# Performance work log

Measured on AMD Instinct MI355X. Metric: run time of the kernel, lower is better.

The kernel has to match this reference:

```python
import jax, jax.numpy as jnp
import numpy as np

GH, GW = 7, 7            # hierarchical grid size
LN_EPS = 1e-5            # torch nn.LayerNorm default eps
NEG = -1e9


def _adaptive_avg_pool2d(x, oh, ow):
    # Replicates torch F.adaptive_avg_pool2d bin boundaries:
    # start=floor(i*H/out), end=ceil((i+1)*H/out). x: (..., H, W)
    H, W = x.shape[-2], x.shape[-1]
    def b(i, n, o):
        return int(np.floor(i * n / o)), int(np.ceil((i + 1) * n / o))
    rows = jnp.stack([x[..., b(i, H, oh)[0]:b(i, H, oh)[1], :].mean(axis=-2)
                      for i in range(oh)], axis=-2)
    out = jnp.stack([rows[..., b(j, W, ow)[0]:b(j, W, ow)[1]].mean(axis=-1)
                     for j in range(ow)], axis=-1)
    return out


def _layernorm(y, gamma, beta):
    mu = y.mean(axis=-1, keepdims=True)
    var = jnp.mean(jnp.square(y - mu), axis=-1, keepdims=True)
    return (y - mu) * jax.lax.rsqrt(var + LN_EPS) * gamma + beta


def setup_inputs() -> dict:
    key = jax.random.key(0)
    ks = jax.random.split(key, 16)
    B, C, H, W = 8, 512, 32, 32
    heads = 8
    s = 0.02
    f32 = jnp.float32
    return {
        "x":    jax.random.normal(ks[0], (B, C, H, W), f32),
        "Wq":   jax.random.normal(ks[1], (C, C), f32) * s,
        "bq":   jnp.zeros((C,), f32),
        "Wk":   jax.random.normal(ks[2], (C, C), f32) * s,
        "bk":   jnp.zeros((C,), f32),
        "Wv":   jax.random.normal(ks[3], (C, C), f32) * s,
        "bv":   jnp.zeros((C,), f32),
        "Wo":   jax.random.normal(ks[4], (C, C), f32) * s,
        "bo":   jnp.zeros((C,), f32),
        "Wsp":  jax.random.normal(ks[5], (heads, C), f32) * s,   # 1x1 conv C->heads
        "bsp":  jnp.zeros((heads,), f32),
        "Wse1": jax.random.normal(ks[6], (C // 16, C), f32) * s, # SE squeeze
        "bse1": jnp.zeros((C // 16,), f32),
        "Wse2": jax.random.normal(ks[7], (C, C // 16), f32) * s, # SE excite
        "bse2": jnp.zeros((C,), f32),
        "gamma": jnp.ones((C,), f32),
        "beta":  jnp.zeros((C,), f32),
    }


def reference(x, Wq, bq, Wk, bk, Wv, bv, Wo, bo, Wsp, bsp,
              Wse1, bse1, Wse2, bse2, gamma, beta):
    B, C, H, W = x.shape
    heads = Wsp.shape[0]
    d = C // heads
    N = H * W

    # --- hierarchical grid mask ---
    sp = jnp.einsum('bchw,nc->bnhw', x, Wsp) + bsp[None, :, None, None]
    m = jax.nn.sigmoid(sp)                               # (B, heads, H, W)
    mg = _adaptive_avg_pool2d(m, GH, GW)
    mg = (mg > 0.5).astype(x.dtype)                      # binarize
    ih = np.floor(np.arange(H) * GH / H).astype(np.int32)  # torch 'nearest'
    iw = np.floor(np.arange(W) * GW / W).astype(np.int32)
    mask = mg[..., ih[:, None], iw[None, :]]             # (B, heads, H, W)

    # --- SE channel gating ---
    pooled = x.mean(axis=(2, 3))                         # (B, C)
    h1 = jax.nn.relu(pooled @ Wse1.T + bse1)
    cw = jax.nn.sigmoid(h1 @ Wse2.T + bse2)              # (B, C)
    xf = (x * cw[:, :, None, None]).reshape(B, C, N).transpose(0, 2, 1)  # (B,N,C)

    # --- multi-head attention with outer-product additive mask ---
    def heads_split(t):
        return t.reshape(B, N, heads, d).transpose(0, 2, 1, 3)  # (B,h,N,d)
    Q = heads_split(xf @ Wq.T + bq)
    K = heads_split(xf @ Wk.T + bk)
    V = heads_split(xf @ Wv.T + bv)

    scores = jnp.einsum('bhnd,bhmd->bhnm', Q, K) / (d ** 0.5)
    mf = mask.reshape(B, heads, N)
    bias = (1.0 - mf[:, :, :, None] * mf[:, :, None, :]) * NEG
    w = jax.nn.softmax(scores + bias, axis=-1)
    attn = jnp.einsum('bhnm,bhmd->bhnd', w, V)
    attn = attn.transpose(0, 2, 1, 3).reshape(B, N, C)
    attn = attn @ Wo.T + bo

    y = _layernorm(xf + attn, gamma, beta)               # (B, N, C)
    return y.transpose(0, 2, 1).reshape(B, C, H, W)
```

## Files before the change

kernel.cpp:

```cpp
#include <hip/hip_runtime.h>
#include <hip/hip_bf16.h>
#include <math.h>

typedef unsigned short u16;
typedef unsigned int u32;
typedef __attribute__((ext_vector_type(4))) float f32x4;
typedef __attribute__((ext_vector_type(8))) short bf16x8;
typedef __attribute__((ext_vector_type(4))) unsigned short us4;
typedef __attribute__((ext_vector_type(8))) unsigned short us8;

#define DI __device__ __forceinline__

#define NEGS  (-1.4426950408889634e9f)
#define QKSCL (0.18033688011112042f)
#define DEFTH (11.541560327111708f)

DI u16 f2b(float x){ __hip_bfloat16 h = __float2bfloat16(x); return *reinterpret_cast<u16*>(&h); }
DI float b2f(u16 u){ union { float f; u32 i; } v; v.i = ((u32)u) << 16; return v.f; }

DI u32 cvtpk(float lo, float hi){
  u32 r;
  asm("v_cvt_pk_bf16_f32 %0, %1, %2" : "=v"(r) : "v"(lo), "v"(hi));
  return r;
}
DI float exp2a(float x){
  float r;
  asm("v_exp_f32 %0, %1" : "=v"(r) : "v"(x));
  return r;
}

DI void gload16(const void* g, void* l){
  __builtin_amdgcn_global_load_lds((const __attribute__((address_space(1))) void*)g,
                                   (__attribute__((address_space(3))) void*)l, 16, 0, 0);
}

__global__ void k_cvt(const float* __restrict__ Wq, const float* __restrict__ Wk,
                      const float* __restrict__ Wv, const float* __restrict__ Wo,
                      u16* __restrict__ WB, u16* __restrict__ WoB){
  int i = blockIdx.x * 256 + threadIdx.x;
  WB[i]          = f2b(Wq[i]);
  WB[262144 + i] = f2b(Wk[i]);
  WB[524288 + i] = f2b(Wv[i]);
  WoB[i]         = f2b(Wo[i]);
}

__global__ __launch_bounds__(256) void k_pooled(const float* __restrict__ x, float* __restrict__ pooled){
  int row  = blockIdx.x * 4 + (threadIdx.x >> 6);
  int lane = threadIdx.x & 63;
  const float4* p = (const float4*)(x + ((size_t)row << 10));
  float4 v0 = p[lane], v1 = p[lane + 64], v2 = p[lane + 128], v3 = p[lane + 192];
  float s = (v0.x + v0.y + v0.z + v0.w) + (v1.x + v1.y + v1.z + v1.w)
          + (v2.x + v2.y + v2.z + v2.w) + (v3.x + v3.y + v3.z + v3.w);
  #pragma unroll
  for (int o = 32; o > 0; o >>= 1) s += __shfl_down(s, o, 64);
  if (lane == 0) pooled[row] = s * (1.0f / 1024.0f);
}

__global__ __launch_bounds__(256) void k_se(const float* __restrict__ pooled,
    const float* __restrict__ Wse1, const float* __restrict__ bse1,
    const float* __restrict__ Wse2, const float* __restrict__ bse2,
    float* __restrict__ cw){
  __shared__ float pl[512];
  __shared__ float h1[32];
  int b = blockIdx.x, t = threadIdx.x;
  pl[t] = pooled[b * 512 + t];
  pl[t + 256] = pooled[b * 512 + t + 256];
  __syncthreads();
  if (t < 32){
    float acc = bse1[t];
    const float* w = Wse1 + t * 512;
    for (int c = 0; c < 512; c++) acc = fmaf(pl[c], w[c], acc);
    h1[t] = fmaxf(acc, 0.0f);
  }
  __syncthreads();
  for (int c = t; c < 512; c += 256){
    float acc = bse2[c];
    const float* w = Wse2 + c * 32;
    #pragma unroll
    for (int j = 0; j < 32; j++) acc = fmaf(h1[j], w[j], acc);
    cw[b * 512 + c] = 1.0f / (1.0f + expf(-acc));
  }
}

__global__ __launch_bounds__(256) void k_spxf(const float* __restrict__ x,
    const float* __restrict__ Wsp, const float* __restrict__ bsp,
    const float* __restrict__ cw, float* __restrict__ mbuf, u16* __restrict__ xfB){
  __shared__ float wsh[4096];
  __shared__ float cwl[512];
  __shared__ float tile[64][36];
  __shared__ float part[8][256];
  int t = threadIdx.x;
  int b = blockIdx.x >> 5, n0 = (blockIdx.x & 31) << 5;
  for (int i = t; i < 4096; i += 256) wsh[i] = Wsp[i];
  cwl[t] = cw[b * 512 + t];
  cwl[t + 256] = cw[b * 512 + t + 256];

  int nl = t & 31, cg = t >> 5;
  int lr = t >> 2, lc = (t & 3) << 3;
  float acc[8] = {0,0,0,0,0,0,0,0};

  for (int cb = 0; cb < 8; cb++){
    __syncthreads();
    const float* xp = x + ((size_t)(b * 512 + cb * 64 + lr) << 10) + n0 + lc;
    float4 v0 = *(const float4*)xp;
    float4 v1 = *(const float4*)(xp + 4);
    *(float4*)&tile[lr][lc]     = v0;
    *(float4*)&tile[lr][lc + 4] = v1;
    __syncthreads();
    float sc[8];
    #pragma unroll
    for (int i = 0; i < 8; i++){
      int c = cb * 64 + cg * 8 + i;
      float v = tile[cg * 8 + i][nl];
      sc[i] = v * cwl[c];
      #pragma unroll
      for (int h = 0; h < 8; h++) acc[h] = fmaf(v, wsh[(h << 9) + c], acc[h]);
    }
    union { u32 d[4]; us8 v; } xu;
    #pragma unroll
    for (int i = 0; i < 4; i++) xu.d[i] = cvtpk(sc[2*i], sc[2*i+1]);
    *(us8*)&xfB[(((size_t)(b * 1024 + n0 + nl)) << 9) + cb * 64 + cg * 8] = xu.v;
  }
  #pragma unroll
  for (int h = 0; h < 8; h++) part[cg][h * 32 + nl] = acc[h];
  __syncthreads();
  {
    int h = t >> 5, px = t & 31;
    float s = bsp[h];
    #pragma unroll
    for (int g2 = 0; g2 < 8; g2++) s += part[g2][h * 32 + px];
    mbuf[(((size_t)(b * 8 + h)) << 10) + n0 + px] = 1.0f / (1.0f + expf(-s));
  }
}

__global__ void k_mask(const float* __restrict__ mbuf, float* __restrict__ bneg){
  __shared__ float sm[1024];
  __shared__ float mg[49];
  int bh = blockIdx.x, t = threadIdx.x;
  const float* mp = mbuf + ((size_t)bh << 10);
  for (int i = t; i < 1024; i += 64) sm[i] = mp[i];
  __syncthreads();
  if (t < 49){
    int ci = t / 7, cj = t % 7;
    int r0 = (ci * 32) / 7, r1 = ((ci + 1) * 32 + 6) / 7;
    int c0 = (cj * 32) / 7, c1 = ((cj + 1) * 32 + 6) / 7;
    float acc = 0.0f;
    for (int cc = c0; cc < c1; cc++){
      float rs = 0.0f;
      for (int rr = r0; rr < r1; rr++) rs += sm[rr * 32 + cc];
      acc += rs / (float)(r1 - r0);
    }
    float v = acc / (float)(c1 - c0);
    mg[t] = (v > 0.5f) ? 1.0f : 0.0f;
  }
  __syncthreads();
  for (int i = t; i < 1024; i += 64){
    int r = i >> 5, c = i & 31;
    float m = mg[((r * 7) >> 5) * 7 + ((c * 7) >> 5)];
    bneg[((size_t)bh << 10) + i] = (m > 0.5f) ? 0.0f : NEGS;
  }
}

template<int MODE>
DI void gemm_body(const u16* __restrict__ A, const u16* __restrict__ Bw,
    const float* __restrict__ b0, const float* __restrict__ b1, const float* __restrict__ b2,
    u16* __restrict__ outQ, u16* __restrict__ outK, u16* __restrict__ outV, u16* __restrict__ outO){
  __shared__ __align__(16) u16 smem[16384];
  int m0 = blockIdx.x * 128, n0 = blockIdx.y * 128;
  bool vblk = (MODE == 0) && (n0 >= 1024);
  int t = threadIdx.x, lane = t & 63, w = t >> 6;
  int wr = w >> 1, wc = w & 1;
  int g = lane >> 4, li = lane & 15;
  f32x4 acc[4][4];
  #pragma unroll
  for (int mt = 0; mt < 4; mt++)
    #pragma unroll
    for (int nt = 0; nt < 4; nt++) acc[mt][nt] = (f32x4){0.f, 0.f, 0.f, 0.f};

  int cof = (((lane & 3) ^ ((lane >> 3) & 3)) << 3);
  int rl = lane >> 2;
  const u16* gA = A  + (size_t)(m0 + w * 32 + rl) * 512 + cof;
  const u16* gB = Bw + (size_t)(n0 + w * 32 + rl) * 512 + cof;
  u16* lA = smem + (w * 32) * 32;
  u16* lB = smem + 4096 + (w * 32) * 32;

  #define STAGE(buf, k0)                                              \
    gload16(gA + (k0),            lA + (buf) * 8192);                 \
    gload16(gA + (k0) + 16 * 512, lA + (buf) * 8192 + 512);           \
    gload16(gB + (k0),            lB + (buf) * 8192);                 \
    gload16(gB + (k0) + 16 * 512, lB + (buf) * 8192 + 512);

  STAGE(0, 0);
  __syncthreads();

  int rsw = ((li >> 1) & 3);
  int cA = (g ^ rsw) << 3;
  int cur = 0;
  for (int ks = 0; ks < 16; ks++){
    if (ks < 15){ STAGE(cur ^ 1, (ks + 1) * 32); }
    const u16* Ac = smem + cur * 8192;
    const u16* Bc = smem + cur * 8192 + 4096;
    bf16x8 afr[4], bfr[4];
    #pragma unroll
    for (int mt = 0; mt < 4; mt++)
      afr[mt] = *(const bf16x8*)&Ac[(wr * 64 + mt * 16 + li) * 32 + cA];
    #pragma unroll
    for (int nt = 0; nt < 4; nt++)
      bfr[nt] = *(const bf16x8*)&Bc[(wc * 64 + nt * 16 + li) * 32 + cA];
    if (vblk){
      #pragma unroll
      for (int mt = 0; mt < 4; mt++)
        #pragma unroll
        for (int nt = 0; nt < 4; nt++)
          acc[mt][nt] = __builtin_amdgcn_mfma_f32_16x16x32_bf16(afr[mt], bfr[nt], acc[mt][nt], 0, 0, 0);
    } else {
      #pragma unroll
      for (int mt = 0; mt < 4; mt++)
        #pragma unroll
        for (int nt = 0; nt < 4; nt++)
          acc[mt][nt] = __builtin_amdgcn_mfma_f32_16x16x32_bf16(bfr[nt], afr[mt], acc[mt][nt], 0, 0, 0);
    }
    __syncthreads();
    cur ^= 1;
  }
  #undef STAGE

  u16* Cl = smem;
  const float* bb = vblk ? b2 : ((MODE == 0 && (n0 >> 9)) ? b1 : b0);
  #pragma unroll
  for (int p = 0; p < 2; p++){
    __syncthreads();
    if (vblk){
      if (wc == p){
        #pragma unroll
        for (int mt = 0; mt < 4; mt++){
          #pragma unroll
          for (int nt = 0; nt < 4; nt++){
            int row = nt * 16 + li;
            float bias = bb[(n0 & 511) + p * 64 + row];
            int col = wr * 64 + ((mt >> 1) << 5) + (g << 3) + ((mt & 1) << 2);
            union { u32 d[2]; us4 v; } pu;
            pu.d[0] = cvtpk(acc[mt][nt][0] + bias, acc[mt][nt][1] + bias);
            pu.d[1] = cvtpk(acc[mt][nt][2] + bias, acc[mt][nt][3] + bias);
            *(us4*)&Cl[row * 136 + col] = pu.v;
          }
        }
      }
    } else {
      if (wr == p){
        #pragma unroll
        for (int mt = 0; mt < 4; mt++){
          #pragma unroll
          for (int nt = 0; nt < 4; nt++){
            int row = mt * 16 + li;
            int ob = wc * 64 + nt * 16 + (g << 2);
            float4 bias4 = *(const float4*)&bb[(n0 & 511) + ob];
            union { u32 d[2]; us4 v; } pu;
            pu.d[0] = cvtpk(acc[mt][nt][0] + bias4.x, acc[mt][nt][1] + bias4.y);
            pu.d[1] = cvtpk(acc[mt][nt][2] + bias4.z, acc[mt][nt][3] + bias4.w);
            *(us4*)&Cl[row * 136 + ob] = pu.v;
          }
        }
      }
    }
    __syncthreads();
    int r = t >> 4, ol = (t & 15) << 3;
    if (vblk){
      int b = m0 >> 10, nt0 = m0 & 1023;
      #pragma unroll
      for (int pp = 0; pp < 4; pp++){
        int rr = pp * 16 + r;
        int c = (n0 & 511) + p * 64 + rr, h = c >> 6, dv = c & 63;
        us8 v = *(us8*)&Cl[rr * 136 + ol];
        *(us8*)&outV[(((size_t)(b * 8 + h)) << 16) + ((size_t)dv << 10) + nt0 + ol] = v;
      }
    } else if (MODE == 0){
      u16* base = (n0 >> 9) ? outK : outQ;
      #pragma unroll
      for (int pp = 0; pp < 4; pp++){
        int rr = pp * 16 + r;
        int m = m0 + p * 64 + rr, b = m >> 10, n = m & 1023;
        int c = (n0 & 511) + ol, h = c >> 6, dv = c & 63;
        us8 v = *(us8*)&Cl[rr * 136 + ol];
        *(us8*)&base[(((size_t)(b * 8 + h)) << 16) + ((size_t)n << 6) + dv] = v;
      }
    } else {
      #pragma unroll
      for (int pp = 0; pp < 4; pp++){
        int rr = pp * 16 + r;
        int m = m0 + p * 64 + rr;
        us8 v = *(us8*)&Cl[rr * 136 + ol];
        *(us8*)&outO[((size_t)m << 9) + n0 + ol] = v;
      }
    }
  }
}

__global__ __launch_bounds__(256) void k_gemm_qkv(const u16* __restrict__ A, const u16* __restrict__ Bw,
    const float* __restrict__ b0, const float* __restrict__ b1, const float* __restrict__ b2,
    u16* __restrict__ outQ, u16* __restrict__ outK, u16* __restrict__ outV){
  gemm_body<0>(A, Bw, b0, b1, b2, outQ, outK, outV, nullptr);
}

__global__ __launch_bounds__(256) void k_gemm_o(const u16* __restrict__ A, const u16* __restrict__ Bw,
    const float* __restrict__ b0, u16* __restrict__ outO){
  gemm_body<1>(A, Bw, b0, nullptr, nullptr, nullptr, nullptr, nullptr, outO);
}

__global__ __launch_bounds__(256) void k_flash(const u16* __restrict__ Q, const u16* __restrict__ K,
    const u16* __restrict__ Vt, const float* __restrict__ bneg, u16* __restrict__ attnB){
  __shared__ __align__(16) u16 Ks[2][64 * 88];
  __shared__ __align__(16) u16 Vts[2][64 * 88];
  __shared__ float mks[2][64];
  int hw = blockIdx.x;
  int bid = ((hw & 7) << 6) + (hw >> 3);
  int bh = bid >> 3, q0 = (bid & 7) << 7;
  int t = threadIdx.x, lane = t & 63, w = t >> 6;
  int g = lane >> 4, li = lane & 15;

  const u16* Kp = K  + ((size_t)bh << 16);
  const u16* Vp = Vt + ((size_t)bh << 16);
  const float* bp = bneg + ((size_t)bh << 10);

  bf16x8 qf0a, qf1a, qf0b, qf1b;
  {
    const u16* qra = Q + ((size_t)bh << 16) + ((size_t)(q0 + w * 32 + li) << 6);
    qf0a = *(const bf16x8*)(qra + g * 8);
    qf1a = *(const bf16x8*)(qra + 32 + g * 8);
    const u16* qrb = qra + (16 << 6);
    qf0b = *(const bf16x8*)(qrb + g * 8);
    qf1b = *(const bf16x8*)(qrb + 32 + g * 8);
  }
  float bnqa = bp[q0 + w * 32 + li];
  float bnqb = bp[q0 + w * 32 + 16 + li];

  f32x4 oaccA[4], oaccB[4];
  #pragma unroll
  for (int dt = 0; dt < 4; dt++){
    oaccA[dt] = (f32x4){0.f, 0.f, 0.f, 0.f};
    oaccB[dt] = (f32x4){0.f, 0.f, 0.f, 0.f};
  }
  float mrunA = -INFINITY, lrunA = 0.0f, mrunB = -INFINITY, lrunB = 0.0f;

  int sr = t >> 2, sc = (t & 3) << 4;
  const u16* kg = Kp + ((size_t)sr << 6) + sc;
  const u16* vg = Vp + ((size_t)sr << 10) + sc;
  uint4 kr0 = *(const uint4*)(kg), kr1 = *(const uint4*)(kg + 8);
  uint4 vr0 = *(const uint4*)(vg), vr1 = *(const uint4*)(vg + 8);
  float mr = (t < 64) ? bp[t] : 0.0f;

  *(uint4*)&Ks[0][sr * 88 + sc]      = kr0;
  *(uint4*)&Ks[0][sr * 88 + sc + 8]  = kr1;
  *(uint4*)&Vts[0][sr * 88 + sc]     = vr0;
  *(uint4*)&Vts[0][sr * 88 + sc + 8] = vr1;
  if (t < 64) mks[0][t] = mr;
  __syncthreads();

  for (int kt = 0; kt < 16; kt++){
    int buf = kt & 1;
    if (kt < 15){
      kr0 = *(const uint4*)(kg + (kt + 1) * 4096);
      kr1 = *(const uint4*)(kg + (kt + 1) * 4096 + 8);
      vr0 = *(const uint4*)(vg + (kt + 1) * 64);
      vr1 = *(const uint4*)(vg + (kt + 1) * 64 + 8);
      if (t < 64) mr = bp[(kt + 1) * 64 + t];
    }

    f32x4 sa[4], sb[4];
    #pragma unroll
    for (int mt = 0; mt < 4; mt++){ sa[mt] = (f32x4){0.f,0.f,0.f,0.f}; sb[mt] = (f32x4){0.f,0.f,0.f,0.f}; }
    __builtin_amdgcn_s_setprio(1);
    #pragma unroll
    for (int mt = 0; mt < 4; mt++){
      bf16x8 kf0 = *(bf16x8*)&Ks[buf][(mt * 16 + li) * 88 + g * 8];
      bf16x8 kf1 = *(bf16x8*)&Ks[buf][(mt * 16 + li) * 88 + 32 + g * 8];
      sa[mt] = __builtin_amdgcn_mfma_f32_16x16x32_bf16(kf0, qf0a, sa[mt], 0, 0, 0);
      sa[mt] = __builtin_amdgcn_mfma_f32_16x16x32_bf16(kf1, qf1a, sa[mt], 0, 0, 0);
      sb[mt] = __builtin_amdgcn_mfma_f32_16x16x32_bf16(kf0, qf0b, sb[mt], 0, 0, 0);
      sb[mt] = __builtin_amdgcn_mfma_f32_16x16x32_bf16(kf1, qf1b, sb[mt], 0, 0, 0);
    }
    __builtin_amdgcn_s_setprio(0);

    union { u32 d[4]; bf16x8 v; } u0a, u1a, u0b, u1b;
    {
      float tm[4];
      #pragma unroll
      for (int mt = 0; mt < 4; mt++){
        float4 bk = *(const float4*)&mks[buf][mt * 16 + g * 4];
        float s0 = fmaf(sa[mt][0], QKSCL, fminf(bk.x, bnqa));
        float s1 = fmaf(sa[mt][1], QKSCL, fminf(bk.y, bnqa));
        float s2 = fmaf(sa[mt][2], QKSCL, fminf(bk.z, bnqa));
        float s3 = fmaf(sa[mt][3], QKSCL, fminf(bk.w, bnqa));
        sa[mt][0] = s0; sa[mt][1] = s1; sa[mt][2] = s2; sa[mt][3] = s3;
        tm[mt] = fmaxf(fmaxf(s0, s1), fmaxf(s2, s3));
      }
      float tmax = fmaxf(fmaxf(tm[0], tm[1]), fmaxf(tm[2], tm[3]));
      tmax = fmaxf(tmax, __shfl_xor(tmax, 16, 64));
      tmax = fmaxf(tmax, __shfl_xor(tmax, 32, 64));
      if (!__all(tmax <= mrunA + DEFTH)){
        float mnew = fmaxf(mrunA, tmax);
        float scl = exp2a(mrunA - mnew);
        mrunA = mnew; lrunA *= scl;
        #pragma unroll
        for (int dt = 0; dt < 4; dt++)
          #pragma unroll
          for (int j = 0; j < 4; j++) oaccA[dt][j] *= scl;
      }
      float rs[4];
      #pragma unroll
      for (int mt = 0; mt < 4; mt++){
        float p0 = exp2a(sa[mt][0] - mrunA);
        float p1 = exp2a(sa[mt][1] - mrunA);
        float p2 = exp2a(sa[mt][2] - mrunA);
        float p3 = exp2a(sa[mt][3] - mrunA);
        sa[mt][0] = p0; sa[mt][1] = p1; sa[mt][2] = p2; sa[mt][3] = p3;
        rs[mt] = (p0 + p1) + (p2 + p3);
      }
      float rsum = (rs[0] + rs[1]) + (rs[2] + rs[3]);
      rsum += __shfl_xor(rsum, 16, 64);
      rsum += __shfl_xor(rsum, 32, 64);
      lrunA += rsum;
      u0a.d[0] = cvtpk(sa[0][0], sa[0][1]); u0a.d[1] = cvtpk(sa[0][2], sa[0][3]);
      u0a.d[2] = cvtpk(sa[1][0], sa[1][1]); u0a.d[3] = cvtpk(sa[1][2], sa[1][3]);
      u1a.d[0] = cvtpk(sa[2][0], sa[2][1]); u1a.d[1] = cvtpk(sa[2][2], sa[2][3]);
      u1a.d[2] = cvtpk(sa[3][0], sa[3][1]); u1a.d[3] = cvtpk(sa[3][2], sa[3][3]);
    }
    {
      float tm[4];
      #pragma unroll
      for (int mt = 0; mt < 4; mt++){
        float4 bk = *(const float4*)&mks[buf][mt * 16 + g * 4];
        float s0 = fmaf(sb[mt][0], QKSCL, fminf(bk.x, bnqb));
        float s1 = fmaf(sb[mt][1], QKSCL, fminf(bk.y, bnqb));
        float s2 = fmaf(sb[mt][2], QKSCL, fminf(bk.z, bnqb));
        float s3 = fmaf(sb[mt][3], QKSCL, fminf(bk.w, bnqb));
        sb[mt][0] = s0; sb[mt][1] = s1; sb[mt][2] = s2; sb[mt][3] = s3;
        tm[mt] = fmaxf(fmaxf(s0, s1), fmaxf(s2, s3));
      }
      float tmax = fmaxf(fmaxf(tm[0], tm[1]), fmaxf(tm[2], tm[3]));
      tmax = fmaxf(tmax, __shfl_xor(tmax, 16, 64));
      tmax = fmaxf(tmax, __shfl_xor(tmax, 32, 64));
      if (!__all(tmax <= mrunB + DEFTH)){
        float mnew = fmaxf(mrunB, tmax);
        float scl = exp2a(mrunB - mnew);
        mrunB = mnew; lrunB *= scl;
        #pragma unroll
        for (int dt = 0; dt < 4; dt++)
          #pragma unroll
          for (int j = 0; j < 4; j++) oaccB[dt][j] *= scl;
      }
      float rs[4];
      #pragma unroll
      for (int mt = 0; mt < 4; mt++){
        float p0 = exp2a(sb[mt][0] - mrunB);
        float p1 = exp2a(sb[mt][1] - mrunB);
        float p2 = exp2a(sb[mt][2] - mrunB);
        float p3 = exp2a(sb[mt][3] - mrunB);
        sb[mt][0] = p0; sb[mt][1] = p1; sb[mt][2] = p2; sb[mt][3] = p3;
        rs[mt] = (p0 + p1) + (p2 + p3);
      }
      float rsum = (rs[0] + rs[1]) + (rs[2] + rs[3]);
      rsum += __shfl_xor(rsum, 16, 64);
      rsum += __shfl_xor(rsum, 32, 64);
      lrunB += rsum;
      u0b.d[0] = cvtpk(sb[0][0], sb[0][1]); u0b.d[1] = cvtpk(sb[0][2], sb[0][3]);
      u0b.d[2] = cvtpk(sb[1][0], sb[1][1]); u0b.d[3] = cvtpk(sb[1][2], sb[1][3]);
      u1b.d[0] = cvtpk(sb[2][0], sb[2][1]); u1b.d[1] = cvtpk(sb[2][2], sb[2][3]);
      u1b.d[2] = cvtpk(sb[3][0], sb[3][1]); u1b.d[3] = cvtpk(sb[3][2], sb[3][3]);
    }

    __builtin_amdgcn_s_setprio(1);
    #pragma unroll
    for (int dt = 0; dt < 4; dt++){
      bf16x8 vf0 = *(bf16x8*)&Vts[buf][(dt * 16 + li) * 88 + g * 8];
      bf16x8 vf1 = *(bf16x8*)&Vts[buf][(dt * 16 + li) * 88 + 32 + g * 8];
      oaccA[dt] = __builtin_amdgcn_mfma_f32_16x16x32_bf16(vf0, u0a.v, oaccA[dt], 0, 0, 0);
      oaccA[dt] = __builtin_amdgcn_mfma_f32_16x16x32_bf16(vf1, u1a.v, oaccA[dt], 0, 0, 0);
      oaccB[dt] = __builtin_amdgcn_mfma_f32_16x16x32_bf16(vf0, u0b.v, oaccB[dt], 0, 0, 0);
      oaccB[dt] = __builtin_amdgcn_mfma_f32_16x16x32_bf16(vf1, u1b.v, oaccB[dt], 0, 0, 0);
    }
    __builtin_amdgcn_s_setprio(0);

    if (kt < 15){
      int nb = buf ^ 1;
      *(uint4*)&Ks[nb][sr * 88 + sc]      = kr0;
      *(uint4*)&Ks[nb][sr * 88 + sc + 8]  = kr1;
      *(uint4*)&Vts[nb][sr * 88 + sc]     = vr0;
      *(uint4*)&Vts[nb][sr * 88 + sc + 8] = vr1;
      if (t < 64) mks[nb][t] = mr;
      __syncthreads();
    }
  }

  int b = bh >> 3, h = bh & 7;
  float invA = 1.0f / lrunA, invB = 1.0f / lrunB;
  u16* opA = attnB + (((size_t)(b * 1024 + q0 + w * 32 + li)) << 9) + h * 64 + g * 4;
  u16* opB = opA + (16 << 9);
  #pragma unroll
  for (int dt = 0; dt < 4; dt++){
    union { u32 d[2]; us4 v; } oa, ob;
    oa.d[0] = cvtpk(oaccA[dt][0] * invA, oaccA[dt][1] * invA);
    oa.d[1] = cvtpk(oaccA[dt][2] * invA, oaccA[dt][3] * invA);
    ob.d[0] = cvtpk(oaccB[dt][0] * invB, oaccB[dt][1] * invB);
    ob.d[1] = cvtpk(oaccB[dt][2] * invB, oaccB[dt][3] * invB);
    *(us4*)(opA + dt * 16) = oa.v;
    *(us4*)(opB + dt * 16) = ob.v;
  }
}

__global__ __launch_bounds__(256) void k_ln(const u16* __restrict__ xfB, const u16* __restrict__ attnO,
    const float* __restrict__ gamma, const float* __restrict__ beta, float* __restrict__ out){
  __shared__ float mu_s[64], rs_s[64];
  __shared__ float tile[64][65];
  int b = blockIdx.x >> 4, n0 = (blockIdx.x & 15) << 6;
  int t = threadIdx.x, w = t >> 6, lane = t & 63;

  for (int r = w * 16; r < w * 16 + 16; r++){
    size_t rb = ((size_t)(b * 1024 + n0 + r)) << 9;
    union { uint4 v; u16 u[8]; } av; av.v = *(const uint4*)(attnO + rb + lane * 8);
    union { uint4 v; u16 u[8]; } xv; xv.v = *(const uint4*)(xfB + rb + lane * 8);
    float s = 0.0f, s2 = 0.0f;
    #pragma unroll
    for (int i = 0; i < 8; i++){
      float v = b2f(av.u[i]) + b2f(xv.u[i]);
      s += v; s2 += v * v;
    }
    #pragma unroll
    for (int o = 32; o > 0; o >>= 1){ s += __shfl_xor(s, o, 64); s2 += __shfl_xor(s2, o, 64); }
    if (lane == 0){
      float mu = s * (1.0f / 512.0f);
      float var = s2 * (1.0f / 512.0f) - mu * mu;
      mu_s[r] = mu;
      rs_s[r] = 1.0f / sqrtf(var + 1e-5f);
    }
  }
  __syncthreads();

  for (int ch = 0; ch < 8; ch++){
    int c0 = ch * 64;
    {
      int r = t >> 2, cp = (t & 3) << 4;
      size_t rb = (((size_t)(b * 1024 + n0 + r)) << 9) + c0 + cp;
      float mu = mu_s[r], rstd = rs_s[r];
      #pragma unroll
      for (int i2 = 0; i2 < 2; i2++){
        union { uint4 v; u16 u[8]; } av; av.v = *(const uint4*)(attnO + rb + i2 * 8);
        union { uint4 v; u16 u[8]; } xv; xv.v = *(const uint4*)(xfB + rb + i2 * 8);
        #pragma unroll
        for (int i = 0; i < 8; i++){
          int c = c0 + cp + i2 * 8 + i;
          float v = b2f(av.u[i]) + b2f(xv.u[i]);
          tile[r][cp + i2 * 8 + i] = (v - mu) * rstd * gamma[c] + beta[c];
        }
      }
    }
    __syncthreads();
    {
      int cl = t >> 2, np_ = (t & 3) << 4;
      float* op = out + (((size_t)(b * 512 + c0 + cl)) << 10) + n0 + np_;
      #pragma unroll
      for (int i = 0; i < 16; i += 4){
        float4 vo = { tile[np_ + i][cl], tile[np_ + i + 1][cl], tile[np_ + i + 2][cl], tile[np_ + i + 3][cl] };
        *(float4*)(op + i) = vo;
      }
    }
    __syncthreads();
  }
}

extern "C" void kernel_launch(void* const* d_in, const int* in_sizes, int n_in,
                              void* d_out, int out_size, void* d_ws, size_t ws_size,
                              hipStream_t stream){
  (void)in_sizes; (void)n_in; (void)out_size; (void)ws_size;
  const float* x    = (const float*)d_in[0];
  const float* Wq   = (const float*)d_in[1];
  const float* bq   = (const float*)d_in[2];
  const float* Wk   = (const float*)d_in[3];
  const float* bk   = (const float*)d_in[4];
  const float* Wv   = (const float*)d_in[5];
  const float* bv   = (const float*)d_in[6];
  const float* Wo   = (const float*)d_in[7];
  const float* bo   = (const float*)d_in[8];
  const float* Wsp  = (const float*)d_in[9];
  const float* bsp  = (const float*)d_in[10];
  const float* Wse1 = (const float*)d_in[11];
  const float* bse1 = (const float*)d_in[12];
  const float* Wse2 = (const float*)d_in[13];
  const float* bse2 = (const float*)d_in[14];
  const float* gamma= (const float*)d_in[15];
  const float* beta = (const float*)d_in[16];
  float* out = (float*)d_out;

  char* ws = (char*)d_ws;
  size_t off = 0;
  auto alloc = [&](size_t bytes) -> void* {
    void* p = ws + off;
    off += (bytes + 255) & ~(size_t)255;
    return p;
  };
  u16*   WB     = (u16*)  alloc(1536 * 512 * 2);
  u16*   WoB    = (u16*)  alloc(512 * 512 * 2);
  float* pooled = (float*)alloc(4096 * 4);
  float* cw     = (float*)alloc(4096 * 4);
  float* mbuf   = (float*)alloc(65536 * 4);
  float* bneg   = (float*)alloc(65536 * 4);
  u16*   xfB    = (u16*)  alloc((size_t)8192 * 512 * 2);
  u16*   Qb     = (u16*)  alloc(8388608);
  u16*   Kb     = (u16*)  alloc(8388608);
  u16*   VtG    = (u16*)  alloc(8388608);
  u16*   attnB  = (u16*)  alloc(8388608);
  u16*   attnOb = Qb;

  k_cvt   <<<dim3(1024), dim3(256), 0, stream>>>(Wq, Wk, Wv, Wo, WB, WoB);
  k_pooled<<<dim3(1024), dim3(256), 0, stream>>>(x, pooled);
  k_se    <<<dim3(8),    dim3(256), 0, stream>>>(pooled, Wse1, bse1, Wse2, bse2, cw);
  k_spxf  <<<dim3(256),  dim3(256), 0, stream>>>(x, Wsp, bsp, cw, mbuf, xfB);
  k_mask  <<<dim3(64),   dim3(64),  0, stream>>>(mbuf, bneg);
  k_gemm_qkv<<<dim3(64, 12), dim3(256), 0, stream>>>(xfB, WB, bq, bk, bv, Qb, Kb, VtG);
  k_flash <<<dim3(512),  dim3(256), 0, stream>>>(Qb, Kb, VtG, bneg, attnB);
  k_gemm_o<<<dim3(64, 4), dim3(256), 0, stream>>>(attnB, WoB, bo, attnOb);
  k_ln    <<<dim3(128),  dim3(256), 0, stream>>>(xfB, attnOb, gamma, beta, out);
}
```

Baseline: 141.7 us.

## Merge weight-convert and pooling kernels, add GEMM occupancy hints, halve LN tile

Combines the weight bf16 conversion and the spatial mean pooling into one launch by splitting the block range, removing one kernel launch. Adds a minimum-blocks-per-CU hint of 4 to both GEMM kernels, which pushes the compiler toward fewer registers and risks spills. Shrinks the LayerNorm tile from 64 to 32 rows so twice as many blocks are launched, improving occupancy across CUs at the cost of shorter per-thread stores.

After: 202.2 us. 42.7% more time.

```diff
diff --git a/kernel.cpp b/kernel.cpp
--- a/kernel.cpp
+++ b/kernel.cpp
@@ -34,26 +34,27 @@
                                    (__attribute__((address_space(3))) void*)l, 16, 0, 0);
 }
 
-__global__ void k_cvt(const float* __restrict__ Wq, const float* __restrict__ Wk,
-                      const float* __restrict__ Wv, const float* __restrict__ Wo,
-                      u16* __restrict__ WB, u16* __restrict__ WoB){
-  int i = blockIdx.x * 256 + threadIdx.x;
-  WB[i]          = f2b(Wq[i]);
-  WB[262144 + i] = f2b(Wk[i]);
-  WB[524288 + i] = f2b(Wv[i]);
-  WoB[i]         = f2b(Wo[i]);
-}
-
-__global__ __launch_bounds__(256) void k_pooled(const float* __restrict__ x, float* __restrict__ pooled){
-  int row  = blockIdx.x * 4 + (threadIdx.x >> 6);
-  int lane = threadIdx.x & 63;
-  const float4* p = (const float4*)(x + ((size_t)row << 10));
-  float4 v0 = p[lane], v1 = p[lane + 64], v2 = p[lane + 128], v3 = p[lane + 192];
-  float s = (v0.x + v0.y + v0.z + v0.w) + (v1.x + v1.y + v1.z + v1.w)
-          + (v2.x + v2.y + v2.z + v2.w) + (v3.x + v3.y + v3.z + v3.w);
-  #pragma unroll
-  for (int o = 32; o > 0; o >>= 1) s += __shfl_down(s, o, 64);
-  if (lane == 0) pooled[row] = s * (1.0f / 1024.0f);
+__global__ __launch_bounds__(256) void k_prep(const float* __restrict__ Wq, const float* __restrict__ Wk,
+    const float* __restrict__ Wv, const float* __restrict__ Wo,
+    u16* __restrict__ WB, u16* __restrict__ WoB,
+    const float* __restrict__ x, float* __restrict__ pooled){
+  if (blockIdx.x < 1024){
+    int i = blockIdx.x * 256 + threadIdx.x;
+    WB[i]          = f2b(Wq[i]);
+    WB[262144 + i] = f2b(Wk[i]);
+    WB[524288 + i] = f2b(Wv[i]);
+    WoB[i]         = f2b(Wo[i]);
+  } else {
+    int row  = (blockIdx.x - 1024) * 4 + (threadIdx.x >> 6);
+    int lane = threadIdx.x & 63;
+    const float4* p = (const float4*)(x + ((size_t)row << 10));
+    float4 v0 = p[lane], v1 = p[lane + 64], v2 = p[lane + 128], v3 = p[lane + 192];
+    float s = (v0.x + v0.y + v0.z + v0.w) + (v1.x + v1.y + v1.z + v1.w)
+            + (v2.x + v2.y + v2.z + v2.w) + (v3.x + v3.y + v3.z + v3.w);
+    #pragma unroll
+    for (int o = 32; o > 0; o >>= 1) s += __shfl_down(s, o, 64);
+    if (lane == 0) pooled[row] = s * (1.0f / 1024.0f);
+  }
 }
 
 __global__ __launch_bounds__(256) void k_se(const float* __restrict__ pooled,
@@ -296,13 +297,13 @@
   }
 }
 
-__global__ __launch_bounds__(256) void k_gemm_qkv(const u16* __restrict__ A, const u16* __restrict__ Bw,
+__global__ __launch_bounds__(256, 4) void k_gemm_qkv(const u16* __restrict__ A, const u16* __restrict__ Bw,
     const float* __restrict__ b0, const float* __restrict__ b1, const float* __restrict__ b2,
     u16* __restrict__ outQ, u16* __restrict__ outK, u16* __restrict__ outV){
   gemm_body<0>(A, Bw, b0, b1, b2, outQ, outK, outV, nullptr);
 }
 
-__global__ __launch_bounds__(256) void k_gemm_o(const u16* __restrict__ A, const u16* __restrict__ Bw,
+__global__ __launch_bounds__(256, 4) void k_gemm_o(const u16* __restrict__ A, const u16* __restrict__ Bw,
     const float* __restrict__ b0, u16* __restrict__ outO){
   gemm_body<1>(A, Bw, b0, nullptr, nullptr, nullptr, nullptr, nullptr, outO);
 }
@@ -510,12 +511,12 @@
 
 __global__ __launch_bounds__(256) void k_ln(const u16* __restrict__ xfB, const u16* __restrict__ attnO,
     const float* __restrict__ gamma, const float* __restrict__ beta, float* __restrict__ out){
-  __shared__ float mu_s[64], rs_s[64];
-  __shared__ float tile[64][65];
-  int b = blockIdx.x >> 4, n0 = (blockIdx.x & 15) << 6;
+  __shared__ float mu_s[32], rs_s[32];
+  __shared__ float tile[32][65];
+  int b = blockIdx.x >> 5, n0 = (blockIdx.x & 31) << 5;
   int t = threadIdx.x, w = t >> 6, lane = t & 63;
 
-  for (int r = w * 16; r < w * 16 + 16; r++){
+  for (int r = w * 8; r < w * 8 + 8; r++){
     size_t rb = ((size_t)(b * 1024 + n0 + r)) << 9;
     union { uint4 v; u16 u[8]; } av; av.v = *(const uint4*)(attnO + rb + lane * 8);
     union { uint4 v; u16 u[8]; } xv; xv.v = *(const uint4*)(xfB + rb + lane * 8);
@@ -539,30 +540,26 @@
   for (int ch = 0; ch < 8; ch++){
     int c0 = ch * 64;
     {
-      int r = t >> 2, cp = (t & 3) << 4;
+      int r = t >> 3, cp = (t & 7) << 3;
       size_t rb = (((size_t)(b * 1024 + n0 + r)) << 9) + c0 + cp;
       float mu = mu_s[r], rstd = rs_s[r];
-      #pragma unroll
-      for (int i2 = 0; i2 < 2; i2++){
-        union { uint4 v; u16 u[8]; } av; av.v = *(const uint4*)(attnO + rb + i2 * 8);
-        union { uint4 v; u16 u[8]; } xv; xv.v = *(const uint4*)(xfB + rb + i2 * 8);
-        #pragma unroll
-        for (int i = 0; i < 8; i++){
-          int c = c0 + cp + i2 * 8 + i;
-          float v = b2f(av.u[i]) + b2f(xv.u[i]);
-          tile[r][cp + i2 * 8 + i] = (v - mu) * rstd * gamma[c] + beta[c];
-        }
+      union { uint4 v; u16 u[8]; } av; av.v = *(const uint4*)(attnO + rb);
+      union { uint4 v; u16 u[8]; } xv; xv.v = *(const uint4*)(xfB + rb);
+      #pragma unroll
+      for (int i = 0; i < 8; i++){
+        int c = c0 + cp + i;
+        float v = b2f(av.u[i]) + b2f(xv.u[i]);
+        tile[r][cp + i] = (v - mu) * rstd * gamma[c] + beta[c];
       }
     }
     __syncthreads();
     {
-      int cl = t >> 2, np_ = (t & 3) << 4;
+      int cl = t >> 2, np_ = (t & 3) << 3;
       float* op = out + (((size_t)(b * 512 + c0 + cl)) << 10) + n0 + np_;
-      #pragma unroll
-      for (int i = 0; i < 16; i += 4){
-        float4 vo = { tile[np_ + i][cl], tile[np_ + i + 1][cl], tile[np_ + i + 2][cl], tile[np_ + i + 3][cl] };
-        *(float4*)(op + i) = vo;
-      }
+      float4 v0 = { tile[np_ + 0][cl], tile[np_ + 1][cl], tile[np_ + 2][cl], tile[np_ + 3][cl] };
+      float4 v1 = { tile[np_ + 4][cl], tile[np_ + 5][cl], tile[np_ + 6][cl], tile[np_ + 7][cl] };
+      *(float4*)op = v0;
+      *(float4*)(op + 4) = v1;
     }
     __syncthreads();
   }
@@ -611,13 +608,12 @@
   u16*   attnB  = (u16*)  alloc(8388608);
   u16*   attnOb = Qb;
 
-  k_cvt   <<<dim3(1024), dim3(256), 0, stream>>>(Wq, Wk, Wv, Wo, WB, WoB);
-  k_pooled<<<dim3(1024), dim3(256), 0, stream>>>(x, pooled);
+  k_prep  <<<dim3(2048), dim3(256), 0, stream>>>(Wq, Wk, Wv, Wo, WB, WoB, x, pooled);
   k_se    <<<dim3(8),    dim3(256), 0, stream>>>(pooled, Wse1, bse1, Wse2, bse2, cw);
   k_spxf  <<<dim3(256),  dim3(256), 0, stream>>>(x, Wsp, bsp, cw, mbuf, xfB);
   k_mask  <<<dim3(64),   dim3(64),  0, stream>>>(mbuf, bneg);
   k_gemm_qkv<<<dim3(64, 12), dim3(256), 0, stream>>>(xfB, WB, bq, bk, bv, Qb, Kb, VtG);
   k_flash <<<dim3(512),  dim3(256), 0, stream>>>(Qb, Kb, VtG, bneg, attnB);
   k_gemm_o<<<dim3(64, 4), dim3(256), 0, stream>>>(attnB, WoB, bo, attnOb);
-  k_ln    <<<dim3(128),  dim3(256), 0, stream>>>(xfB, attnOb, gamma, beta, out);
-}
+  k_ln    <<<dim3(256),  dim3(256), 0, stream>>>(xfB, attnOb, gamma, beta, out);
+}
```
